# Kernel optimization log

Hardware: AMD Instinct MI355X
Metric: run time of the kernel (lower is better)

The kernel has to match this reference:

```python
import jax, jax.numpy as jnp
from jax import lax
import numpy as np

H, W = 2048, 2048
MAXN = 100
THR, BOXTHR, SIZETHR, MAR = 0.3, 0.7, 5.0, 1.0


def _label(msk):
    # Connected-component labeling via iterative 3x3 max propagation + LUT path compression.
    Hh, Ww = msk.shape
    flat = msk.reshape(-1).astype(jnp.int32)
    # row-major labels 1..num_pixels on foreground, 0 on background (matches torch arange assignment)
    lab = (jnp.cumsum(flat) * flat).reshape(Hh, Ww)
    N = Hh * Ww
    lut = jnp.arange(N + 1, dtype=jnp.int32)
    for s in (12, 6, 3):
        # labels are >= 0, so init 0 matches torch max_pool2d (-inf pad) semantics here
        maxlab = lax.reduce_window(lab, jnp.int32(0), lax.max, (3, 3), (1, 1), 'SAME')
        upd = maxlab > lab
        idx = jnp.where(upd, lab, 0).reshape(-1)
        val = jnp.where(upd, maxlab, 0).reshape(-1)
        lut = lut.at[idx].max(val)
        lut = lut.at[0].set(0)
        for _ in range(s):
            lut = lut[lut]  # path compression
        lab = lut[lab]
    # relabel to consecutive ids sorted by label value (== torch.unique return_inverse)
    present = jnp.zeros(N + 1, jnp.int32).at[lab.reshape(-1)].set(1)
    ranks = jnp.cumsum(present) - 1
    return ranks[lab]


def _svd_2d(var_x, cov_xy, var_y):
    theta = 0.5 * jnp.arctan2(2.0 * cov_xy, var_x - var_y)
    c, s = jnp.cos(theta), jnp.sin(theta)
    rot = jnp.stack([jnp.stack([c, -s], -1), jnp.stack([s, c], -1)], -2)  # [n,2,2]
    trace = var_x + var_y
    disc = jnp.maximum((var_x - var_y) ** 2 + 4.0 * cov_xy ** 2, 1e-12)
    sq = jnp.sqrt(disc)
    l1 = jnp.maximum((trace + sq) * 0.5, 0.0)
    l2 = jnp.maximum((trace - sq) * 0.5, 0.0)
    return rot, jnp.sqrt(jnp.stack([l1, l2], -1))  # [n,2,2], [n,2]


def _bbox(hot):
    lab = _label(hot > THR)
    lab = jnp.where(lab >= MAXN, 0, lab).reshape(-1)  # [P]
    ys, xs = jnp.meshgrid(jnp.arange(hot.shape[0]), jnp.arange(hot.shape[1]), indexing='ij')
    xf = xs.reshape(-1).astype(jnp.float32)
    yf = ys.reshape(-1).astype(jnp.float32)
    ss = lambda w: jax.ops.segment_sum(w, lab, num_segments=MAXN)
    area = ss(jnp.ones_like(xf))
    mu_x = ss(xf) / area
    mu_y = ss(yf) / area
    cx = xf - mu_x[lab]
    cy = yf - mu_y[lab]
    xx = ss(cx * cx) / area
    xy = ss(cx * cy) / area
    yy = ss(cy * cy) / area
    m, l = _svd_2d(xx, xy, yy)
    margin = jnp.sqrt(l[:, 1]) * 4.0 * MAR
    coords = jnp.stack([cx, cy], -1)  # centered coords, [P,2]
    rxy = jnp.einsum('pji,pj->pi', m[lab], coords)  # m^T @ coords per pixel
    # torch scatter_reduce amin/amax with include_self=True over zero-init buffer -> clamp vs 0
    smin = lambda w: jnp.minimum(jax.ops.segment_min(w, lab, num_segments=MAXN), 0.0)
    smax = lambda w: jnp.maximum(jax.ops.segment_max(w, lab, num_segments=MAXN), 0.0)
    minx = smin(rxy[:, 0]) - margin
    maxx = smax(rxy[:, 0]) + margin
    miny = smin(rxy[:, 1]) - margin
    maxy = smax(rxy[:, 1]) + margin
    recs = jnp.stack([minx, miny, maxx, miny, maxx, maxy, minx, maxy, minx, miny], -1)
    recs = recs.reshape(-1, 5, 2).transpose(0, 2, 1)  # [n,2,5]
    mu_xy = jnp.stack([mu_x, mu_y], -1)  # [n,2]
    newxy = (jnp.einsum('nij,njk->nik', m, recs) + mu_xy[:, :, None]).transpose(0, 2, 1)  # [n,5,2]
    level = ss(hot.reshape(-1))
    msk = (level / area > BOXTHR) & (maxx - minx > SIZETHR) & (maxy - miny > SIZETHR)
    return newxy, msk


def setup_inputs() -> dict:
    key = jax.random.key(0)
    k1, k2 = jax.random.split(key)
    hot = jax.random.uniform(k1, (H, W), dtype=jnp.float32)
    scale = jax.random.uniform(k2, (1,), dtype=jnp.float32) + 0.5
    return {'hot': hot, 'scale': scale}


def reference(hot, scale):
    newxy, msk = _bbox(hot)
    # fixed-shape masked output [MAXN,5,2] instead of data-dependent boolean filtering
    sel = jnp.where(msk[:, None, None], newxy, 0.0)
    return sel * scale * 2.0
```

## Files before the change

kernel.cpp:

```cpp
#include <hip/hip_runtime.h>
#include <math.h>

#define HH 2048
#define WW 2048
#define NPIX (HH*WW)
#define NP4  (NPIX/4)
#define MAXNC 100

#define S_AREA 0
#define S_SHOT 300
#define S_MUX  400
#define S_MUY  500
#define S_RC   900
#define S_RS   1000
#define S_MG   1100
#define S_KMINX 1200
#define S_KMAXX 1300
#define S_KMINY 1400
#define S_KMAXY 1500
#define S_TOT  1600

__device__ __forceinline__ unsigned int encf(float f){
  unsigned int u = __float_as_uint(f);
  return (u & 0x80000000u) ? ~u : (u | 0x80000000u);
}
__device__ __forceinline__ float decf(unsigned int k){
  return (k & 0x80000000u) ? __uint_as_float(k & 0x7fffffffu) : __uint_as_float(~k);
}

__device__ __forceinline__ int xcd_swz(int b, int nwg){
  int q = nwg >> 3, r = nwg & 7;
  int xcd = b & 7, o = b >> 3;
  return (xcd < r ? xcd*(q+1) : r*(q+1) + (xcd-r)*q) + o;
}

__device__ __forceinline__ float blockReduceSum(float v, float* sh){
  int t = threadIdx.x;
  __syncthreads();
  sh[t] = v; __syncthreads();
  for (int o = 128; o > 0; o >>= 1){ if (t < o) sh[t] += sh[t+o]; __syncthreads(); }
  float r = sh[0]; __syncthreads();
  return r;
}
__device__ __forceinline__ double blockReduceSumD(double v, double* sh){
  int t = threadIdx.x;
  __syncthreads();
  sh[t] = v; __syncthreads();
  for (int o = 128; o > 0; o >>= 1){ if (t < o) sh[t] += sh[t+o]; __syncthreads(); }
  double r = sh[0]; __syncthreads();
  return r;
}
__device__ __forceinline__ float blockReduceMin(float v, float* sh){
  int t = threadIdx.x;
  __syncthreads();
  sh[t] = v; __syncthreads();
  for (int o = 128; o > 0; o >>= 1){ if (t < o) sh[t] = fminf(sh[t], sh[t+o]); __syncthreads(); }
  float r = sh[0]; __syncthreads();
  return r;
}
__device__ __forceinline__ float blockReduceMax(float v, float* sh){
  int t = threadIdx.x;
  __syncthreads();
  sh[t] = v; __syncthreads();
  for (int o = 128; o > 0; o >>= 1){ if (t < o) sh[t] = fmaxf(sh[t], sh[t+o]); __syncthreads(); }
  float r = sh[0]; __syncthreads();
  return r;
}


template<bool R1>
__global__ __launch_bounds__(256) void k_scatter_row(const float* __restrict__ hot,
                                                     const int* __restrict__ lab,
                                                     int* __restrict__ lut){
  int y  = xcd_swz(blockIdx.x, HH);
  int t  = threadIdx.x;
  int x0 = t << 3;
  int P  = (y << 11) + x0;
  int ci = t << 1;
  int cim = (ci > 0) ? ci - 1 : 0;
  int rows3[3];
  rows3[0] = (y > 0) ? y-1 : 0;
  rows3[1] = y;
  rows3[2] = (y < HH-1) ? y+1 : HH-1;

  int c[3][10];
  #pragma unroll
  for (int j = 0; j < 3; ++j){
    int rb = rows3[j] << 9;
    if constexpr (R1){
      const float4* h4 = (const float4*)hot;
      float4 a = h4[rb + cim], b = h4[rb + ci], d = h4[rb + ci + 1];
      int lb = rows3[j]*WW + (x0 - 2) + 1;
      c[j][0] = (a.z > 0.3f) ? lb   : 0;
      c[j][1] = (a.w > 0.3f) ? lb+1 : 0;
      c[j][2] = (b.x > 0.3f) ? lb+2 : 0;
      c[j][3] = (b.y > 0.3f) ? lb+3 : 0;
      c[j][4] = (b.z > 0.3f) ? lb+4 : 0;
      c[j][5] = (b.w > 0.3f) ? lb+5 : 0;
      c[j][6] = (d.x > 0.3f) ? lb+6 : 0;
      c[j][7] = (d.y > 0.3f) ? lb+7 : 0;
      c[j][8] = (d.z > 0.3f) ? lb+8 : 0;
      c[j][9] = (d.w > 0.3f) ? lb+9 : 0;
    } else {
      const int4* l4 = (const int4*)lab;
      int4 a = l4[rb + cim], b = l4[rb + ci], d = l4[rb + ci + 1];
      c[j][0] = a.z; c[j][1] = a.w;
      c[j][2] = b.x; c[j][3] = b.y; c[j][4] = b.z; c[j][5] = b.w;
      c[j][6] = d.x; c[j][7] = d.y; c[j][8] = d.z; c[j][9] = d.w;
    }
    if (t == 0){ c[j][0] = c[j][2]; c[j][1] = c[j][2]; }
  }

  int m[8];
  #pragma unroll
  for (int k = 0; k < 8; ++k){
    int h0 = max(max(c[0][k], c[0][k+1]), c[0][k+2]);
    int h1 = max(max(c[1][k], c[1][k+1]), c[1][k+2]);
    int h2 = max(max(c[2][k], c[2][k+1]), c[2][k+2]);
    m[k] = max(h0, max(h1, h2));
  }

  if constexpr (R1){
    int val[8];
    #pragma unroll
    for (int k = 0; k < 8; ++k){
      int l = c[1][k+1];
      val[k] = l ? m[k] : (P + k);
    }
    if (t == 0){
      if (y == 0) val[0] = 0;
      else {
        int rr0 = (y >= 2) ? y-2 : 0;
        int rr[3] = {rr0, y-1, y};
        int mm = 0;
        #pragma unroll
        for (int j = 0; j < 3; ++j){
          float ha = hot[rr[j]*WW + 2046], hb = hot[rr[j]*WW + 2047];
          int la  = (ha > 0.3f) ? rr[j]*WW + 2047 : 0;
          int lbv = (hb > 0.3f) ? rr[j]*WW + 2048 : 0;
          mm = max(mm, max(la, lbv));
        }
        bool fgq = hot[(y-1)*WW + 2047] > 0.3f;
        val[0] = fgq ? mm : P;
      }
    }
    *(int4*)(lut + P)     = make_int4(val[0], val[1], val[2], val[3]);
    *(int4*)(lut + P + 4) = make_int4(val[4], val[5], val[6], val[7]);
    if (y == HH-1 && t == 255){
      int mm = max(max(c[0][8], c[0][9]), max(c[1][8], c[1][9]));
      int l = c[1][9];
      lut[NPIX] = l ? mm : NPIX;
    }
  } else {
    #pragma unroll
    for (int k = 0; k < 8; ++k){
      if (t == 0 && k == 0) continue;
      int l = c[1][k+1];
      if (l != 0 && m[k] > l) atomicMax(&lut[l], m[k]);
    }
    if (t == 0 && y > 0){
      int q = P - 1;
      int l = lab[q];
      if (l != 0){
        int rr0 = (y >= 2) ? y-2 : 0;
        int rr[3] = {rr0, y-1, y};
        int mm = 0;
        #pragma unroll
        for (int j = 0; j < 3; ++j)
          mm = max(mm, max(lab[rr[j]*WW + 2046], lab[rr[j]*WW + 2047]));
        if (mm > l) atomicMax(&lut[l], mm);
      }
    }
    if (y == HH-1 && t == 255){
      int mm = max(max(c[0][8], c[0][9]), max(c[1][8], c[1][9]));
      int l = c[1][9];
      if (l != 0 && mm > l) atomicMax(&lut[l], mm);
    }
  }
}

template<int HOPS>
__global__ void k_compress(const int* __restrict__ src, int* __restrict__ dst){
  int wb = xcd_swz(blockIdx.x, gridDim.x);
  int base = (wb*256 + threadIdx.x) * 4;
  if (base + 3 <= NPIX){
    int4 v = *(const int4*)(src + base);
    int j0 = v.x, j1 = v.y, j2 = v.z, j3 = v.w;
    #pragma unroll 1
    for (int k = 0; k < HOPS; ++k){
      int n0 = src[j0], n1 = src[j1], n2 = src[j2], n3 = src[j3];
      bool done = (n0==j0) && (n1==j1) && (n2==j2) && (n3==j3);
      j0 = n0; j1 = n1; j2 = n2; j3 = n3;
      if (done) break;
    }
    *(int4*)(dst + base) = make_int4(j0, j1, j2, j3);
  } else {
    for (int i = base; i <= NPIX; ++i){
      int j = src[i];
      for (int k = 0; k < HOPS; ++k){
        int n = src[j];
        if (n == j) break;
        j = n;
      }
      dst[i] = j;
    }
  }
}

__global__ void k_apply1(const float* __restrict__ hot, const int* __restrict__ lut,
                         int* __restrict__ lab){
  int t = xcd_swz(blockIdx.x, gridDim.x)*256 + threadIdx.x;
  if (t >= NP4) return;
  float4 h = ((const float4*)hot)[t];
  int4 A = ((const int4*)lut)[t];
  int nb = lut[4*t + 4];
  int4 L;
  L.x = (h.x > 0.3f) ? A.y : 0;
  L.y = (h.y > 0.3f) ? A.z : 0;
  L.z = (h.z > 0.3f) ? A.w : 0;
  L.w = (h.w > 0.3f) ? nb  : 0;
  ((int4*)lab)[t] = L;
}

__global__ void k_apply_clear(int* __restrict__ lab, const int* __restrict__ lut,
                              int* __restrict__ presw){
  int rid = blockIdx.x*256 + threadIdx.x;
  if (rid < NP4) presw[rid] = 0;
  if (rid == 0) ((unsigned char*)presw)[NPIX] = 0;
  int t = xcd_swz(blockIdx.x, gridDim.x)*256 + threadIdx.x;
  if (t >= NP4) return;
  int4 L = ((int4*)lab)[t];
  L.x = lut[L.x]; L.y = lut[L.y]; L.z = lut[L.z]; L.w = lut[L.w];
  ((int4*)lab)[t] = L;
}

__global__ void k_chase_mark(int* __restrict__ lab, const int* __restrict__ lut,
                             unsigned char* __restrict__ presb){
  int t = blockIdx.x*256 + threadIdx.x;
  if (t >= NP4) return;
  int4 L = ((int4*)lab)[t];
  int j0 = L.x, j1 = L.y, j2 = L.z, j3 = L.w;
  #pragma unroll 1
  for (int k = 0; k < 8; ++k){
    int n0 = lut[j0], n1 = lut[j1], n2 = lut[j2], n3 = lut[j3];
    bool done = (n0==j0) && (n1==j1) && (n2==j2) && (n3==j3);
    j0 = n0; j1 = n1; j2 = n2; j3 = n3;
    if (done) break;
  }
  ((int4*)lab)[t] = make_int4(j0, j1, j2, j3);
  presb[j0] = 1; presb[j1] = 1; presb[j2] = 1; presb[j3] = 1;
}


__global__ void k_scan1(const unsigned char* __restrict__ presb, int* __restrict__ bsum){
  __shared__ int sh[256];
  int t = threadIdx.x;
  int base = blockIdx.x*4096 + t*16;
  int run = 0;
  if (base + 15 <= NPIX){
    int4 v = *(const int4*)(presb + base);
    run = (int)((((unsigned)v.x & 0x01010101u) * 0x01010101u) >> 24)
        + (int)((((unsigned)v.y & 0x01010101u) * 0x01010101u) >> 24)
        + (int)((((unsigned)v.z & 0x01010101u) * 0x01010101u) >> 24)
        + (int)((((unsigned)v.w & 0x01010101u) * 0x01010101u) >> 24);
  } else {
    for (int k = 0; k < 16; ++k){ int idx = base + k; if (idx <= NPIX) run += presb[idx]; }
  }
  sh[t] = run; __syncthreads();
  for (int o = 128; o > 0; o >>= 1){ if (t < o) sh[t] += sh[t+o]; __syncthreads(); }
  if (t == 0) bsum[blockIdx.x] = sh[0];
}

__global__ void k_scan2(int* __restrict__ bs, int nb, float* __restrict__ st){
  __shared__ int sh[1024];
  int t = threadIdx.x;
  for (int idx = t; idx < S_TOT + 1000; idx += 1024){
    st[idx] = (idx >= S_KMINX && idx < S_TOT) ? -0.0f : 0.0f;
  }
  int v = (t < nb) ? bs[t] : 0;
  sh[t] = v; __syncthreads();
  for (int o = 1; o < 1024; o <<= 1){
    int add = (t >= o) ? sh[t-o] : 0;
    __syncthreads();
    sh[t] += add;
    __syncthreads();
  }
  if (t < nb) bs[t] = (t == 0) ? 0 : sh[t-1];
  if (t == 1023 && nb > 1024) bs[1024] = sh[1023];
}

__global__ void k_scan3(const unsigned char* __restrict__ presb,
                        const int* __restrict__ bsum, int* __restrict__ ranks){
  __shared__ int sh[256];
  int t = threadIdx.x;
  int base = blockIdx.x*4096 + t*16;
  int v[16];
  int run = 0;
  bool vec = (base + 15 <= NPIX);
  if (vec){
    int4 q = *(const int4*)(presb + base);
    unsigned w[4] = {(unsigned)q.x, (unsigned)q.y, (unsigned)q.z, (unsigned)q.w};
    #pragma unroll
    for (int a = 0; a < 4; ++a){
      #pragma unroll
      for (int bb = 0; bb < 4; ++bb){ run += (w[a] >> (8*bb)) & 1; v[a*4+bb] = run; }
    }
  } else {
    for (int k = 0; k < 16; ++k){
      int idx = base + k;
      int x = (idx <= NPIX) ? presb[idx] : 0;
      run += x; v[k] = run;
    }
  }
  sh[t] = run; __syncthreads();
  for (int o = 1; o < 256; o <<= 1){
    int add = (t >= o) ? sh[t-o] : 0;
    __syncthreads();
    sh[t] += add;
    __syncthreads();
  }
  int offs = bsum[blockIdx.x] + sh[t] - run - 1;
  if (vec){
    int4* r4 = (int4*)(ranks + base);
    #pragma unroll
    for (int k = 0; k < 4; ++k)
      r4[k] = make_int4(v[4*k]+offs, v[4*k+1]+offs, v[4*k+2]+offs, v[4*k+3]+offs);
  } else {
    for (int k = 0; k < 16; ++k){ int idx = base + k; if (idx <= NPIX) ranks[idx] = v[k] + offs; }
  }
}


__global__ void k_statsA(int* __restrict__ lab, const int* __restrict__ ranks,
                         const float* __restrict__ hot, float* __restrict__ st,
                         double* __restrict__ sd){
  __shared__ float shf[256];
  __shared__ double shd[256];
  float  n0 = 0.f, h0 = 0.f;
  double sx0 = 0.0, sy0 = 0.0, sxx0 = 0.0, sxy0 = 0.0, syy0 = 0.0;
  int stride = gridDim.x * blockDim.x;
  for (int t = blockIdx.x*blockDim.x + threadIdx.x; t < NP4; t += stride){
    int4 L = ((int4*)lab)[t];
    float4 hq = ((const float4*)hot)[t];
    int p0 = t*4;
    float xb = (float)(p0 & (WW-1));
    double yd = (double)(p0 >> 11);
    int ls[4] = {L.x, L.y, L.z, L.w};
    float hs[4] = {hq.x, hq.y, hq.z, hq.w};
    #pragma unroll
    for (int j = 0; j < 4; ++j){
      int r = ranks[ls[j]];
      int s = (r >= MAXNC) ? 0 : r;
      ls[j] = s;
      double xd = (double)(xb + (float)j);
      if (s == 0){
        n0 += 1.f; h0 += hs[j];
        sx0 += xd; sy0 += yd;
        sxx0 += xd*xd; sxy0 += xd*yd; syy0 += yd*yd;
      } else {
        atomicAdd(&st[S_AREA+s], 1.f);
        atomicAdd(&st[S_SHOT+s], hs[j]);
        atomicAdd(&sd[s],       xd);
        atomicAdd(&sd[100+s],   yd);
        atomicAdd(&sd[200+s],   xd*xd);
        atomicAdd(&sd[300+s],   xd*yd);
        atomicAdd(&sd[400+s],   yd*yd);
      }
    }
    ((int4*)lab)[t] = make_int4(ls[0], ls[1], ls[2], ls[3]);
  }
  n0   = blockReduceSum(n0, shf);
  h0   = blockReduceSum(h0, shf);
  sx0  = blockReduceSumD(sx0, shd);
  sy0  = blockReduceSumD(sy0, shd);
  sxx0 = blockReduceSumD(sxx0, shd);
  sxy0 = blockReduceSumD(sxy0, shd);
  syy0 = blockReduceSumD(syy0, shd);
  if (threadIdx.x == 0){
    atomicAdd(&st[S_AREA], n0);
    atomicAdd(&st[S_SHOT], h0);
    atomicAdd(&sd[0],   sx0);
    atomicAdd(&sd[100], sy0);
    atomicAdd(&sd[200], sxx0);
    atomicAdd(&sd[300], sxy0);
    atomicAdd(&sd[400], syy0);
  }
}

__global__ void k_svd2(float* __restrict__ st, const double* __restrict__ sd){
  int s = threadIdx.x;
  if (s >= MAXNC) return;
  float  n  = st[S_AREA+s];
  double nd = (double)n;
  double sx = sd[s], sy = sd[100+s];
  double mux = sx/nd, muy = sy/nd;
  st[S_MUX+s] = (float)mux;
  st[S_MUY+s] = (float)muy;
  float vx  = (float)(sd[200+s]/nd - mux*mux);
  float vxy = (float)(sd[300+s]/nd - mux*muy);
  float vy  = (float)(sd[400+s]/nd - muy*muy);
  float theta = 0.5f * atan2f(2.0f*vxy, vx - vy);
  float c = cosf(theta), sn = sinf(theta);
  float tr = vx + vy;
  float d = (vx - vy)*(vx - vy) + 4.0f*vxy*vxy;
  float disc = fmaxf(d, 1e-12f);
  float sq = sqrtf(disc);
  float l2 = fmaxf((tr - sq)*0.5f, 0.0f);
  float margin = sqrtf(sqrtf(l2)) * 4.0f;
  st[S_RC+s] = c;
  st[S_RS+s] = sn;
  st[S_MG+s] = margin;
}

__global__ void k_stats3(const int* __restrict__ lab, float* __restrict__ st){
  __shared__ float sh[256];
  unsigned int* ku = (unsigned int*)st;
  float mnx =  INFINITY, mxx = -INFINITY, mny =  INFINITY, mxy = -INFINITY;
  int stride = gridDim.x * blockDim.x;
  for (int t = blockIdx.x*blockDim.x + threadIdx.x; t < NP4; t += stride){
    int4 L = ((int4*)lab)[t];
    int p0 = t*4;
    float xb = (float)(p0 & (WW-1));
    float yf = (float)(p0 >> 11);
    int ls[4] = {L.x, L.y, L.z, L.w};
    #pragma unroll
    for (int j = 0; j < 4; ++j){
      int s = ls[j];
      float cx = xb + (float)j - st[S_MUX+s];
      float cy = yf - st[S_MUY+s];
      float c = st[S_RC+s], sn = st[S_RS+s];
      float rx =  c*cx + sn*cy;
      float ry = -sn*cx + c*cy;
      if (s == 0){
        mnx = fminf(mnx, rx); mxx = fmaxf(mxx, rx);
        mny = fminf(mny, ry); mxy = fmaxf(mxy, ry);
      } else {
        atomicMin(&ku[S_KMINX+s], encf(rx));
        atomicMax(&ku[S_KMAXX+s], encf(rx));
        atomicMin(&ku[S_KMINY+s], encf(ry));
        atomicMax(&ku[S_KMAXY+s], encf(ry));
      }
    }
  }
  mnx = blockReduceMin(mnx, sh);
  mxx = blockReduceMax(mxx, sh);
  mny = blockReduceMin(mny, sh);
  mxy = blockReduceMax(mxy, sh);
  if (threadIdx.x == 0){
    atomicMin(&ku[S_KMINX], encf(mnx));
    atomicMax(&ku[S_KMAXX], encf(mxx));
    atomicMin(&ku[S_KMINY], encf(mny));
    atomicMax(&ku[S_KMAXY], encf(mxy));
  }
}

__global__ void k_final(const float* __restrict__ st, const float* __restrict__ scale, float* __restrict__ out){
  int s = threadIdx.x;
  if (s >= MAXNC) return;
  const unsigned int* ku = (const unsigned int*)st;
  float a   = st[S_AREA+s];
  float lvl = st[S_SHOT+s];
  float mg  = st[S_MG+s];
  float minx = decf(ku[S_KMINX+s]) - mg;
  float maxx = decf(ku[S_KMAXX+s]) + mg;
  float miny = decf(ku[S_KMINY+s]) - mg;
  float maxy = decf(ku[S_KMAXY+s]) + mg;
  bool ok = (lvl/a > 0.7f) && (maxx - minx > 5.0f) && (maxy - miny > 5.0f);
  float c = st[S_RC+s], sn = st[S_RS+s];
  float mux = st[S_MUX+s], muy = st[S_MUY+s];
  float sc2 = scale[0] * 2.0f;
  float rxs[5] = {minx, maxx, maxx, minx, minx};
  float rys[5] = {miny, miny, maxy, maxy, miny};
  #pragma unroll
  for (int k = 0; k < 5; ++k){
    float X = c*rxs[k] - sn*rys[k] + mux;
    float Y = sn*rxs[k] + c*rys[k] + muy;
    out[s*10 + 2*k + 0] = ok ? X * sc2 : 0.0f;
    out[s*10 + 2*k + 1] = ok ? Y * sc2 : 0.0f;
  }
}


extern "C" void kernel_launch(void* const* d_in, const int* in_sizes, int n_in,
                              void* d_out, int out_size, void* d_ws, size_t ws_size,
                              hipStream_t stream) {
  const float* hot   = (const float*)d_in[0];
  const float* scale = (const float*)d_in[1];
  float* out = (float*)d_out;

  char* ws = (char*)d_ws;
  size_t off = 0;
  int* lab  = (int*)(ws + off); off += (size_t)NPIX * 4;
  int* lutA = (int*)(ws + off); off += (size_t)(NPIX + 64) * 4;
  int* lutB = (int*)(ws + off); off += (size_t)(NPIX + 64) * 4;
  int* bsum = (int*)(ws + off); off += 2048 * 4;
  float* st = (float*)(ws + off); off += (S_TOT + 1000) * 4;
  double* sd = (double*)(st + S_TOT);

  dim3 B(256);
  int g4  = (NP4 + 255) / 256;
  int g4t = (NP4 + 256) / 256;
  int NB  = (NPIX + 1 + 4095) / 4096;

  int* cur = lutA;
  int* alt = lutB;

  k_scatter_row<true ><<<HH, B, 0, stream>>>(hot, lab, cur);
  for (int i = 0; i < 6; ++i){
    k_compress<3><<<g4t, B, 0, stream>>>(cur, alt);
    int* tp = cur; cur = alt; alt = tp;
  }
  k_apply1<<<g4, B, 0, stream>>>(hot, cur, lab);

  k_scatter_row<false><<<HH, B, 0, stream>>>(hot, lab, cur);
  for (int i = 0; i < 3; ++i){
    k_compress<3><<<g4t, B, 0, stream>>>(cur, alt);
    int* tp = cur; cur = alt; alt = tp;
  }
  unsigned char* presb = (unsigned char*)alt;
  k_apply_clear<<<g4, B, 0, stream>>>(lab, cur, (int*)presb);

  k_scatter_row<false><<<HH, B, 0, stream>>>(hot, lab, cur);
  k_chase_mark<<<g4, B, 0, stream>>>(lab, cur, presb);

  int* ranks = cur;
  k_scan1<<<NB, B, 0, stream>>>(presb, bsum);
  k_scan2<<<1, 1024, 0, stream>>>(bsum, NB, st);
  k_scan3<<<NB, B, 0, stream>>>(presb, bsum, ranks);

  k_statsA<<<2048, B, 0, stream>>>(lab, ranks, hot, st, sd);
  k_svd2<<<1, 128, 0, stream>>>(st, sd);
  k_stats3<<<2048, B, 0, stream>>>(lab, st);
  k_final<<<1, 128, 0, stream>>>(st, scale, out);
}
```

Before: 362.4 us.

## Fuse label apply with scatter and keep merge edges in a separate buffer

Adds a path that uses a separate edge buffer E for atomicMax merges instead of writing into the LUT. Label application is fused with the second neighbor-max scatter through a shared-memory row tile, and label lookup is fused with the third scatter. The compress and chase kernels now take the max of LUT and E on each hop, and buffer clears are folded into compress and scatter kernels. This removes several full-image passes and kernel launches but needs extra workspace, does more loads per hop, and changes the propagation semantics.

```diff
diff --git a/kernel.cpp b/kernel.cpp
--- a/kernel.cpp
+++ b/kernel.cpp
@@ -179,8 +179,13 @@
   }
 }
 
-template<int HOPS>
-__global__ void k_compress(const int* __restrict__ src, int* __restrict__ dst){
+template<int HOPS, bool CLR>
+__global__ void k_compress(const int* __restrict__ src, int* __restrict__ dst,
+                           int* __restrict__ clrbuf){
+  if (CLR){
+    int ridx = blockIdx.x*256 + threadIdx.x;
+    if (ridx < (NPIX+64)/4) ((int4*)clrbuf)[ridx] = make_int4(0,0,0,0);
+  }
   int wb = xcd_swz(blockIdx.x, gridDim.x);
   int base = (wb*256 + threadIdx.x) * 4;
   if (base + 3 <= NPIX){
@@ -206,6 +211,159 @@
     }
   }
 }
+
+template<int HOPS>
+__global__ void k_compress_mx(const int* __restrict__ A, const int* __restrict__ E,
+                              int* __restrict__ dst){
+  int wb = xcd_swz(blockIdx.x, gridDim.x);
+  int base = (wb*256 + threadIdx.x) * 4;
+  if (base + 3 <= NPIX){
+    int4 a = *(const int4*)(A + base);
+    int4 e = *(const int4*)(E + base);
+    int j0 = max(a.x,e.x), j1 = max(a.y,e.y), j2 = max(a.z,e.z), j3 = max(a.w,e.w);
+    #pragma unroll 1
+    for (int k = 0; k < HOPS; ++k){
+      int n0 = max(A[j0], E[j0]), n1 = max(A[j1], E[j1]);
+      int n2 = max(A[j2], E[j2]), n3 = max(A[j3], E[j3]);
+      bool done = (n0==j0) && (n1==j1) && (n2==j2) && (n3==j3);
+      j0 = n0; j1 = n1; j2 = n2; j3 = n3;
+      if (done) break;
+    }
+    *(int4*)(dst + base) = make_int4(j0, j1, j2, j3);
+  } else {
+    for (int i = base; i <= NPIX; ++i){
+      int j = max(A[i], E[i]);
+      for (int k = 0; k < HOPS; ++k){
+        int n = max(A[j], E[j]);
+        if (n == j) break;
+        j = n;
+      }
+      dst[i] = j;
+    }
+  }
+}
+
+__global__ __launch_bounds__(256) void k_apply1_scat2(const float* __restrict__ hot,
+                                                      const int* __restrict__ lutA,
+                                                      int* __restrict__ lab,
+                                                      int* __restrict__ E){
+  __shared__ int sh[6*2048];
+  int b  = xcd_swz(blockIdx.x, 512);
+  int r0 = b << 2;
+  int t  = threadIdx.x;
+  int x0 = t << 3;
+  #pragma unroll
+  for (int j = 0; j < 6; ++j){
+    int rg = r0 - 1 + j; rg = rg < 0 ? 0 : (rg > HH-1 ? HH-1 : rg);
+    const float4* h4 = (const float4*)(hot + (rg<<11));
+    float4 ha = h4[t*2], hb = h4[t*2+1];
+    int i0 = (rg<<9) + t*2;
+    const int4* A4 = (const int4*)lutA;
+    int4 u = A4[i0], v = A4[i0+1], w = A4[i0+2];
+    int4 o0, o1;
+    o0.x = (ha.x > 0.3f) ? u.y : 0;
+    o0.y = (ha.y > 0.3f) ? u.z : 0;
+    o0.z = (ha.z > 0.3f) ? u.w : 0;
+    o0.w = (ha.w > 0.3f) ? v.x : 0;
+    o1.x = (hb.x > 0.3f) ? v.y : 0;
+    o1.y = (hb.y > 0.3f) ? v.z : 0;
+    o1.z = (hb.z > 0.3f) ? v.w : 0;
+    o1.w = (hb.w > 0.3f) ? w.x : 0;
+    ((int4*)sh)[(j<<9) + t*2]     = o0;
+    ((int4*)sh)[(j<<9) + t*2 + 1] = o1;
+  }
+  __syncthreads();
+  #pragma unroll
+  for (int k = 0; k < 4; ++k){
+    int4* d = (int4*)(lab + ((r0+k)<<11));
+    d[t*2]   = ((int4*)sh)[((k+1)<<9) + t*2];
+    d[t*2+1] = ((int4*)sh)[((k+1)<<9) + t*2 + 1];
+  }
+  #pragma unroll
+  for (int i = 0; i < 8; ++i){
+    int x  = t + (i<<8);
+    int xm = (x > 0) ? x-1 : 0;
+    int xp = (x < WW-1) ? x+1 : WW-1;
+    int h[6], c[6];
+    #pragma unroll
+    for (int j = 0; j < 6; ++j){
+      int a0 = sh[(j<<11)+xm], a1 = sh[(j<<11)+x], a2 = sh[(j<<11)+xp];
+      h[j] = max(max(a0,a1),a2);
+      c[j] = a1;
+    }
+    #pragma unroll
+    for (int k = 0; k < 4; ++k){
+      int m = max(h[k], max(h[k+1], h[k+2]));
+      int l = c[k+1];
+      if (l != 0 && m > l) atomicMax(&E[l], m);
+    }
+  }
+}
+
+__global__ __launch_bounds__(256) void k_scat3b(const int* __restrict__ lab,
+                                                const int* __restrict__ lutB,
+                                                int* __restrict__ E,
+                                                int* __restrict__ presw){
+  __shared__ int sh[6*2048];
+  int t = threadIdx.x;
+  {
+    int rawslice = blockIdx.x * 512;
+    int4* p4 = (int4*)presw;
+    p4[rawslice + t]       = make_int4(0,0,0,0);
+    p4[rawslice + t + 256] = make_int4(0,0,0,0);
+    if (blockIdx.x == 0 && t == 0) ((unsigned char*)presw)[NPIX] = 0;
+  }
+  int b  = xcd_swz(blockIdx.x, 512);
+  int r0 = b << 2;
+  #pragma unroll
+  for (int j = 0; j < 6; ++j){
+    int rg = r0 - 1 + j; rg = rg < 0 ? 0 : (rg > HH-1 ? HH-1 : rg);
+    const int4* l4 = (const int4*)(lab + (rg<<11));
+    int4 a = l4[t*2], c2 = l4[t*2+1];
+    ((int4*)sh)[(j<<9) + t*2]     = make_int4(lutB[a.x],  lutB[a.y],  lutB[a.z],  lutB[a.w]);
+    ((int4*)sh)[(j<<9) + t*2 + 1] = make_int4(lutB[c2.x], lutB[c2.y], lutB[c2.z], lutB[c2.w]);
+  }
+  __syncthreads();
+  #pragma unroll
+  for (int i = 0; i < 8; ++i){
+    int x  = t + (i<<8);
+    int xm = (x > 0) ? x-1 : 0;
+    int xp = (x < WW-1) ? x+1 : WW-1;
+    int h[6], c[6];
+    #pragma unroll
+    for (int j = 0; j < 6; ++j){
+      int a0 = sh[(j<<11)+xm], a1 = sh[(j<<11)+x], a2 = sh[(j<<11)+xp];
+      h[j] = max(max(a0,a1),a2);
+      c[j] = a1;
+    }
+    #pragma unroll
+    for (int k = 0; k < 4; ++k){
+      int m = max(h[k], max(h[k+1], h[k+2]));
+      int l = c[k+1];
+      if (l != 0 && m > l) atomicMax(&E[l], m);
+    }
+  }
+}
+
+__global__ void k_chase_mark2(int* __restrict__ lab, const int* __restrict__ lutB,
+                              const int* __restrict__ E,
+                              unsigned char* __restrict__ presb){
+  int t = blockIdx.x*256 + threadIdx.x;
+  if (t >= NP4) return;
+  int4 L = ((int4*)lab)[t];
+  int j0 = lutB[L.x], j1 = lutB[L.y], j2 = lutB[L.z], j3 = lutB[L.w];
+  #pragma unroll 1
+  for (int k = 0; k < 8; ++k){
+    int n0 = max(lutB[j0], E[j0]), n1 = max(lutB[j1], E[j1]);
+    int n2 = max(lutB[j2], E[j2]), n3 = max(lutB[j3], E[j3]);
+    bool done = (n0==j0) && (n1==j1) && (n2==j2) && (n3==j3);
+    j0 = n0; j1 = n1; j2 = n2; j3 = n3;
+    if (done) break;
+  }
+  ((int4*)lab)[t] = make_int4(j0, j1, j2, j3);
+  presb[j0] = 1; presb[j1] = 1; presb[j2] = 1; presb[j3] = 1;
+}
+
 
 __global__ void k_apply1(const float* __restrict__ hot, const int* __restrict__ lut,
                          int* __restrict__ lab){
@@ -496,6 +654,9 @@
   int* bsum = (int*)(ws + off); off += 2048 * 4;
   float* st = (float*)(ws + off); off += (S_TOT + 1000) * 4;
   double* sd = (double*)(st + S_TOT);
+  int* E = (int*)(ws + off);
+  size_t need = off + (size_t)(NPIX + 64) * 4;
+  bool fused = (ws_size >= need);
 
   dim3 B(256);
   int g4  = (NP4 + 255) / 256;
@@ -507,21 +668,35 @@
 
   k_scatter_row<true ><<<HH, B, 0, stream>>>(hot, lab, cur);
   for (int i = 0; i < 6; ++i){
-    k_compress<3><<<g4t, B, 0, stream>>>(cur, alt);
+    if (fused && i == 5) k_compress<3,true ><<<g4t, B, 0, stream>>>(cur, alt, E);
+    else                 k_compress<3,false><<<g4t, B, 0, stream>>>(cur, alt, nullptr);
     int* tp = cur; cur = alt; alt = tp;
   }
-  k_apply1<<<g4, B, 0, stream>>>(hot, cur, lab);
-
-  k_scatter_row<false><<<HH, B, 0, stream>>>(hot, lab, cur);
-  for (int i = 0; i < 3; ++i){
-    k_compress<3><<<g4t, B, 0, stream>>>(cur, alt);
-    int* tp = cur; cur = alt; alt = tp;
-  }
-  unsigned char* presb = (unsigned char*)alt;
-  k_apply_clear<<<g4, B, 0, stream>>>(lab, cur, (int*)presb);
-
-  k_scatter_row<false><<<HH, B, 0, stream>>>(hot, lab, cur);
-  k_chase_mark<<<g4, B, 0, stream>>>(lab, cur, presb);
+
+  unsigned char* presb;
+  if (fused){
+    k_apply1_scat2<<<512, B, 0, stream>>>(hot, cur, lab, E);
+    k_compress_mx<3><<<g4t, B, 0, stream>>>(cur, E, alt);
+    { int* tp = cur; cur = alt; alt = tp; }
+    k_compress<3,true ><<<g4t, B, 0, stream>>>(cur, alt, E);
+    { int* tp = cur; cur = alt; alt = tp; }
+    k_compress<3,false><<<g4t, B, 0, stream>>>(cur, alt, nullptr);
+    { int* tp = cur; cur = alt; alt = tp; }
+    presb = (unsigned char*)alt;
+    k_scat3b<<<512, B, 0, stream>>>(lab, cur, E, (int*)presb);
+    k_chase_mark2<<<g4, B, 0, stream>>>(lab, cur, E, presb);
+  } else {
+    k_apply1<<<g4, B, 0, stream>>>(hot, cur, lab);
+    k_scatter_row<false><<<HH, B, 0, stream>>>(hot, lab, cur);
+    for (int i = 0; i < 3; ++i){
+      k_compress<3,false><<<g4t, B, 0, stream>>>(cur, alt, nullptr);
+      int* tp = cur; cur = alt; alt = tp;
+    }
+    presb = (unsigned char*)alt;
+    k_apply_clear<<<g4, B, 0, stream>>>(lab, cur, (int*)presb);
+    k_scatter_row<false><<<HH, B, 0, stream>>>(hot, lab, cur);
+    k_chase_mark<<<g4, B, 0, stream>>>(lab, cur, presb);
+  }
 
   int* ranks = cur;
   k_scan1<<<NB, B, 0, stream>>>(presb, bsum);
```

After: 397.1 us. 1.1x slower.
